# Kernel tuning notes

Hardware: AMD Instinct MI355X
Metric: run time of the kernel (lower is better)

The kernel has to match this reference:

```python
import jax, jax.numpy as jnp
import numpy as np

B, D, H = 8192, 256, 1024


def setup_inputs() -> dict:
    key = jax.random.key(0)
    ks = jax.random.split(key, 24)
    glorot = lambda k, o, i: jax.random.uniform(k, (o, i), jnp.float32, -1.0, 1.0) * jnp.sqrt(6.0 / (o + i))
    inp = {
        'x': jax.random.normal(ks[0], (B, D), jnp.float32),
        'm': (jax.random.uniform(ks[1], (B, D)) < 0.8).astype(jnp.float32),  # binary observation mask
        'delta': jax.random.uniform(ks[2], (B, D), jnp.float32),             # nonnegative time gaps
        'h': jax.random.normal(ks[3], (B, H), jnp.float32),
        'x_last_obs': jax.random.normal(ks[4], (B, D), jnp.float32),
        'x_mean': jax.random.normal(ks[5], (D,), jnp.float32),
        'W_gamma_x': jax.random.uniform(ks[6], (D,), jnp.float32, 0.001, 0.01),
        'b_gamma_x': jnp.zeros((D,), jnp.float32),
        'W_gamma_h': glorot(ks[7], H, D), 'b_gamma_h': jnp.zeros((H,), jnp.float32),
        'W_xz': glorot(ks[8], H, D), 'W_hz': glorot(ks[9], H, H),
        'W_mz': glorot(ks[10], H, D), 'b_mz': jnp.zeros((H,), jnp.float32),
        'W_xr': glorot(ks[11], H, D), 'W_hr': glorot(ks[12], H, H),
        'W_mr': glorot(ks[13], H, D), 'b_mr': jnp.zeros((H,), jnp.float32),
        'W_xh': glorot(ks[14], H, D), 'W_hh': glorot(ks[15], H, H),
        'W_mh': glorot(ks[16], H, D), 'b_mh': jnp.zeros((H,), jnp.float32),
    }
    return inp


def reference(x, m, delta, h, x_last_obs, x_mean,
              W_gamma_x, b_gamma_x, W_gamma_h, b_gamma_h,
              W_xz, W_hz, W_mz, b_mz,
              W_xr, W_hr, W_mr, b_mr,
              W_xh, W_hh, W_mh, b_mh):
    # input decay (per-feature) and hidden decay (linear of delta)
    gamma_x = jnp.exp(-jax.nn.relu(delta * W_gamma_x + b_gamma_x))        # [B, D]
    gamma_h = jnp.exp(-jax.nn.relu(delta @ W_gamma_h.T + b_gamma_h))     # [B, H]
    # imputation
    x_last_obs_new = jnp.where(m > 0, x, x_last_obs)
    x_imputed = gamma_x * x_last_obs_new + (1.0 - gamma_x) * x_mean
    x_hat = m * x + (1.0 - m) * x_imputed
    h_decayed = gamma_h * h
    # GRU gates (eval mode: no recurrent dropout)
    z = jax.nn.sigmoid(x_hat @ W_xz.T + h_decayed @ W_hz.T + m @ W_mz.T + b_mz)
    r = jax.nn.sigmoid(x_hat @ W_xr.T + h_decayed @ W_hr.T + m @ W_mr.T + b_mr)
    h_tilde = jnp.tanh(x_hat @ W_xh.T + (r * h_decayed) @ W_hh.T + m @ W_mh.T + b_mh)
    h_new = (1.0 - z) * h_decayed + z * h_tilde
    return h_new, x_last_obs_new
```

## Files before the change

kernel.cpp:

```cpp
#include <hip/hip_runtime.h>
#include <cstdint>
#include <cstddef>

typedef unsigned short u16;
typedef __attribute__((ext_vector_type(8))) short s16x8;
typedef __attribute__((ext_vector_type(8))) u16 u16x8;
typedef __attribute__((ext_vector_type(4))) float f32x4;

#define DEV static __device__ __forceinline__
#define GPTR(p) (const __attribute__((address_space(1))) void*)(p)
#define LPTR(p) (__attribute__((address_space(3))) void*)(p)
#define SCHEDB __builtin_amdgcn_sched_barrier(0)
#define BAR __builtin_amdgcn_s_barrier()
#define SETP1 __builtin_amdgcn_s_setprio(1)
#define SETP0 __builtin_amdgcn_s_setprio(0)

DEV float b2f(u16 u) { union { unsigned i; float f; } c; c.i = ((unsigned)u) << 16; return c.f; }
DEV u16 f2b(float f) {
  union { float f; unsigned i; } c; c.f = f;
  unsigned r = (c.i + 0x7fffu + ((c.i >> 16) & 1u)) >> 16;
  return (u16)r;
}
DEV float sigm(float x) { return 1.0f / (1.0f + __expf(-x)); }

__global__ __launch_bounds__(256) void pack_w(
    const float* __restrict__ Wxz, const float* __restrict__ Whz, const float* __restrict__ Wmz,
    const float* __restrict__ Wxr, const float* __restrict__ Whr, const float* __restrict__ Wmr,
    const float* __restrict__ Wxh, const float* __restrict__ Whh, const float* __restrict__ Wmh,
    const float* __restrict__ Wgh,
    u16* __restrict__ WZR, u16* __restrict__ WH, u16* __restrict__ WGH)
{
  int t = blockIdx.x * 256 + threadIdx.x;
  const float* src;
  u16* dst;
  if (t < 589824) {
    int row = t / 192;
    int col = (t % 192) * 8;
    int rr = row & 1023;
    const float *wx, *wh, *wm;
    if (row < 1024)      { wx = Wxz; wh = Whz; wm = Wmz; }
    else if (row < 2048) { wx = Wxr; wh = Whr; wm = Wmr; }
    else                 { wx = Wxh; wh = Whh; wm = Wmh; }
    if (col < 256)       src = wx + rr * 256 + col;
    else if (col < 1280) src = wh + (size_t)rr * 1024 + (col - 256);
    else                 src = wm + rr * 256 + (col - 1280);
    dst = (row < 2048) ? (WZR + (size_t)row * 1536 + col)
                       : (WH + (size_t)(row - 2048) * 1536 + col);
  } else {
    int t2 = t - 589824;
    src = Wgh + t2 * 8;
    dst = WGH + t2 * 8;
  }
  f32x4 a = *(const f32x4*)src;
  f32x4 b = *(const f32x4*)(src + 4);
  u16x8 v;
#pragma unroll
  for (int j = 0; j < 4; ++j) { v[j] = f2b(a[j]); v[j + 4] = f2b(b[j]); }
  *(u16x8*)dst = v;
}

__global__ __launch_bounds__(256) void elem_k(
    const float* __restrict__ x, const float* __restrict__ m, const float* __restrict__ delta,
    const float* __restrict__ xlo, const float* __restrict__ x_mean,
    const float* __restrict__ Wgx, const float* __restrict__ bgx,
    u16* __restrict__ X1, u16* __restrict__ X2, u16* __restrict__ Dbf,
    float* __restrict__ out_xlo)
{
  int t = blockIdx.x * 256 + threadIdx.x;
  int row = t >> 5;
  int col = (t & 31) * 8;
  size_t base = (size_t)row * 256 + col;
  u16x8 vxhat, vm16, vd16;
  f32x4 vlnew[2];
#pragma unroll
  for (int half = 0; half < 2; ++half) {
    f32x4 vx = *(const f32x4*)(x + base + half * 4);
    f32x4 vm = *(const f32x4*)(m + base + half * 4);
    f32x4 vd = *(const f32x4*)(delta + base + half * 4);
    f32x4 vl = *(const f32x4*)(xlo + base + half * 4);
    f32x4 vmean = *(const f32x4*)(x_mean + col + half * 4);
    f32x4 vwg = *(const f32x4*)(Wgx + col + half * 4);
    f32x4 vbg = *(const f32x4*)(bgx + col + half * 4);
#pragma unroll
    for (int j = 0; j < 4; ++j) {
      float mf = vm[j];
      float lnew = (mf > 0.5f) ? vx[j] : vl[j];
      vlnew[half][j] = lnew;
      float gx = __expf(-fmaxf(vd[j] * vwg[j] + vbg[j], 0.0f));
      float ximp = gx * lnew + (1.0f - gx) * vmean[j];
      float xhat = mf * vx[j] + (1.0f - mf) * ximp;
      vxhat[half * 4 + j] = f2b(xhat);
      vm16[half * 4 + j] = f2b(mf);
      vd16[half * 4 + j] = f2b(vd[j]);
    }
  }
  size_t r1536 = (size_t)row * 1536;
  *(u16x8*)(X1 + r1536 + col) = vxhat;
  *(u16x8*)(X2 + r1536 + col) = vxhat;
  *(u16x8*)(X1 + r1536 + 1280 + col) = vm16;
  *(u16x8*)(X2 + r1536 + 1280 + col) = vm16;
  *(u16x8*)(Dbf + base) = vd16;
  *(f32x4*)(out_xlo + base) = vlnew[0];
  *(f32x4*)(out_xlo + base + 4) = vlnew[1];
}

template<int EPI, int GXL>
__global__ __launch_bounds__(512, 4) void gemm_bt(
    const u16* __restrict__ A, int K, const u16* __restrict__ W,
    const float* __restrict__ bias0, const float* __restrict__ bias1,
    const float* __restrict__ auxf,
    const u16* __restrict__ auxb,
    const u16* __restrict__ aux2b,
    u16* __restrict__ out0b,
    u16* __restrict__ out1b,
    float* __restrict__ outf)
{
  constexpr int GX = 1 << GXL;
  constexpr int SL = 128 * 32;
  __shared__ alignas(16) u16 As[4][SL];
  __shared__ alignas(16) u16 Bs[4][SL];

  const int tid = threadIdx.x;
  const int lane = tid & 63;
  const int wave = tid >> 6;
  const int wr = wave >> 2, wc = wave & 3;

  const int d = blockIdx.x;
  const int q = (int)gridDim.x >> 3;
  const int L = (d & 7) * q + (d >> 3);
  const int brow = (L >> GXL) * 128;
  const int bcol = (L & (GX - 1)) * 128;
  const int NT = K / 64;

  const int lr = lane & 15, g4 = lane >> 4;
  const int rc = (g4 ^ ((lr >> 1) & 3)) * 8;
  const int srow = lane >> 2;
  const int scs = ((lane & 3) ^ ((srow >> 1) & 3)) * 8;

  f32x4 acc[4][2];
#pragma unroll
  for (int i = 0; i < 4; ++i)
#pragma unroll
    for (int j = 0; j < 2; ++j) { f32x4 z0 = {0.f, 0.f, 0.f, 0.f}; acc[i][j] = z0; }

  const u16* aP = A + (size_t)(brow + wave * 16 + srow) * K + scs;
  const u16* bP = W + (size_t)(bcol + wave * 16 + srow) * K + scs;
  u16* ldsA = &As[0][0] + wave * 512;
  u16* ldsB = &Bs[0][0] + wave * 512;
  const u16* rdA = &As[0][0] + (wr * 64 + lr) * 32 + rc;
  const u16* rdB = &Bs[0][0] + (wc * 32 + lr) * 32 + rc;

  auto STAGE = [&](int slot, int koff) {
    __builtin_amdgcn_global_load_lds(GPTR(aP + koff), LPTR(ldsA + slot * SL), 16, 0, 0);
    __builtin_amdgcn_global_load_lds(GPTR(bP + koff), LPTR(ldsB + slot * SL), 16, 0, 0);
  };

  auto PHASE = [&](int slotR, int slotS, int koff, int stg, int vm) {
    s16x8 af[4], bf[2];
    const u16* pA = rdA + slotR * SL;
    const u16* pB = rdB + slotR * SL;
#pragma unroll
    for (int i = 0; i < 4; ++i) af[i] = *(const s16x8*)(pA + i * 512);
#pragma unroll
    for (int j = 0; j < 2; ++j) bf[j] = *(const s16x8*)(pB + j * 512);
    if (stg) STAGE(slotS, koff);
    SCHEDB;
    if (vm == 2) asm volatile("s_waitcnt vmcnt(2)" ::: "memory");
    else if (vm == 0) asm volatile("s_waitcnt vmcnt(0)" ::: "memory");
    BAR;
    asm volatile("s_waitcnt lgkmcnt(0)" ::: "memory");
    SCHEDB;
    SETP1;
#pragma unroll
    for (int i = 0; i < 4; ++i)
#pragma unroll
      for (int j = 0; j < 2; ++j)
        acc[i][j] = __builtin_amdgcn_mfma_f32_16x16x32_bf16(af[i], bf[j], acc[i][j], 0, 0, 0);
    SETP0;
  };

  STAGE(0, 0);
  STAGE(1, 32);
  asm volatile("s_waitcnt vmcnt(2)" ::: "memory");
  BAR;

  for (int kt = 0; kt < NT - 2; kt += 2) {
    PHASE(0, 2, 64, 1, 2);
    PHASE(1, 3, 96, 1, 2);
    PHASE(2, 0, 128, 1, 2);
    PHASE(3, 1, 160, 1, 2);
    aP += 128; bP += 128;
  }
  PHASE(0, 2, 64, 1, 2);
  PHASE(1, 3, 96, 1, 2);
  PHASE(2, 0, 0, 0, 0);
  PHASE(3, 0, 0, 0, -1);

  const int row0 = brow + wr * 64 + g4 * 4;
  const int col0 = bcol + wc * 32 + lr;
#pragma unroll
  for (int i = 0; i < 4; ++i) {
#pragma unroll
    for (int j = 0; j < 2; ++j) {
      int c_ = col0 + j * 16;
#pragma unroll
      for (int qq = 0; qq < 4; ++qq) {
        int r_ = row0 + i * 16 + qq;
        float v = acc[i][j][qq];
        if constexpr (EPI == 0) {
          float p = v + bias0[c_];
          float gh = __expf(-fmaxf(p, 0.0f));
          float hd = gh * auxf[(size_t)r_ * 1024 + c_];
          out0b[(size_t)r_ * 1536 + 256 + c_] = f2b(hd);
        } else if constexpr (EPI == 1) {
          if (c_ < 1024) {
            out0b[(size_t)r_ * 1024 + c_] = f2b(sigm(v + bias0[c_]));
          } else {
            int jc = c_ - 1024;
            float rg = sigm(v + bias1[jc]);
            float hd = b2f(auxb[(size_t)r_ * 1536 + 256 + jc]);
            out1b[(size_t)r_ * 1536 + 256 + jc] = f2b(rg * hd);
          }
        } else {
          float ht = tanhf(v + bias0[c_]);
          float zz = b2f(aux2b[(size_t)r_ * 1024 + c_]);
          float hd = b2f(auxb[(size_t)r_ * 1536 + 256 + c_]);
          outf[(size_t)r_ * 1024 + c_] = (1.0f - zz) * hd + zz * ht;
        }
      }
    }
  }
}

extern "C" void kernel_launch(void* const* d_in, const int* in_sizes, int n_in,
                              void* d_out, int out_size, void* d_ws, size_t ws_size,
                              hipStream_t stream)
{
  const float* x     = (const float*)d_in[0];
  const float* m     = (const float*)d_in[1];
  const float* delta = (const float*)d_in[2];
  const float* h     = (const float*)d_in[3];
  const float* xlo   = (const float*)d_in[4];
  const float* xmean = (const float*)d_in[5];
  const float* Wgx   = (const float*)d_in[6];
  const float* bgx   = (const float*)d_in[7];
  const float* Wgh   = (const float*)d_in[8];
  const float* bgh   = (const float*)d_in[9];
  const float* Wxz   = (const float*)d_in[10];
  const float* Whz   = (const float*)d_in[11];
  const float* Wmz   = (const float*)d_in[12];
  const float* bmz   = (const float*)d_in[13];
  const float* Wxr   = (const float*)d_in[14];
  const float* Whr   = (const float*)d_in[15];
  const float* Wmr   = (const float*)d_in[16];
  const float* bmr   = (const float*)d_in[17];
  const float* Wxh   = (const float*)d_in[18];
  const float* Whh   = (const float*)d_in[19];
  const float* Wmh   = (const float*)d_in[20];
  const float* bmh   = (const float*)d_in[21];

  u16* X1  = (u16*)d_ws;
  u16* X2  = X1 + (size_t)8192 * 1536;
  u16* Z   = X2 + (size_t)8192 * 1536;
  u16* WZR = Z  + (size_t)8192 * 1024;
  u16* WH  = WZR + (size_t)2048 * 1536;
  u16* Dbf = WH + (size_t)1024 * 1536;
  u16* WGH = Dbf + (size_t)8192 * 256;

  float* out_h   = (float*)d_out;
  float* out_xlo = out_h + (size_t)8192 * 1024;

  pack_w<<<2432, 256, 0, stream>>>(Wxz, Whz, Wmz, Wxr, Whr, Wmr, Wxh, Whh, Wmh, Wgh, WZR, WH, WGH);
  elem_k<<<1024, 256, 0, stream>>>(x, m, delta, xlo, xmean, Wgx, bgx, X1, X2, Dbf, out_xlo);
  gemm_bt<0, 3><<<512, 512, 0, stream>>>(
      Dbf, 256, WGH, bgh, nullptr, h, nullptr, nullptr, X1, nullptr, nullptr);
  gemm_bt<1, 4><<<1024, 512, 0, stream>>>(
      X1, 1536, WZR, bmz, bmr, nullptr, X1, nullptr, Z, X2, nullptr);
  gemm_bt<2, 3><<<512, 512, 0, stream>>>(
      X2, 1536, WH, bmh, nullptr, nullptr, X1, Z, nullptr, nullptr, out_h);
}
```

Baseline: 159.8 us.

## Use 256x128 tiles with triple-buffered pipeline for the z/r gate GEMM

Replaces the generic 128x128 gate GEMM (z and r gates, K=1536, N=2048) with a dedicated kernel using 256x128 block tiles, 8 waves each computing a 64x64 sub-tile, a BK=32 triple-buffered direct global-to-LDS load pipeline and one barrier per step. Larger tiles give more MFMA work per loaded byte and halve the grid to 512 blocks. The old EPI==1 path and its extra output parameter are removed. The cost is higher register use (16 accumulators per wave) and a finer K step with more barriers, which could limit occupancy or latency hiding.

Measured after the change: 153.6 us (median of 2 runs). 1.04x faster.

```diff
diff --git a/kernel.cpp b/kernel.cpp
--- a/kernel.cpp
+++ b/kernel.cpp
@@ -104,6 +104,99 @@
   *(f32x4*)(out_xlo + base + 4) = vlnew[1];
 }
 
+__global__ __launch_bounds__(512, 4) void gemm_b256(
+    const u16* __restrict__ A, const u16* __restrict__ W,
+    const float* __restrict__ bz, const float* __restrict__ br,
+    const u16* __restrict__ X1h, u16* __restrict__ Z, u16* __restrict__ X2)
+{
+  constexpr int K = 1536, P = 48;
+  __shared__ alignas(16) u16 As[3][8192];
+  __shared__ alignas(16) u16 Bs[3][4096];
+
+  const int tid = threadIdx.x, lane = tid & 63, wave = tid >> 6;
+  const int wr = wave >> 1, wc = wave & 1;
+  const int d = blockIdx.x;
+  const int L = (d & 7) * 64 + (d >> 3);
+  const int brow = (L >> 4) * 256, bcol = (L & 15) * 128;
+  const int lr = lane & 15, g4 = lane >> 4;
+  const int rc = (g4 ^ ((lr >> 1) & 3)) * 8;
+  const int srow = tid >> 2;
+  const int scs = ((tid & 3) ^ ((srow >> 1) & 3)) * 8;
+
+  f32x4 acc[4][4];
+#pragma unroll
+  for (int i = 0; i < 4; ++i)
+#pragma unroll
+    for (int j = 0; j < 4; ++j) { f32x4 z0 = {0.f, 0.f, 0.f, 0.f}; acc[i][j] = z0; }
+
+  const u16* aP = A + (size_t)(brow + srow) * K + scs;
+  const u16* aQ = aP + (size_t)128 * K;
+  const u16* bP = W + (size_t)(bcol + srow) * K + scs;
+  u16* dA = &As[0][0] + tid * 8;
+  u16* dB = &Bs[0][0] + tid * 8;
+  const u16* rA = &As[0][0] + (wr * 64 + lr) * 32 + rc;
+  const u16* rB = &Bs[0][0] + (wc * 64 + lr) * 32 + rc;
+
+  auto STAGE = [&](int slot, int ko) {
+    __builtin_amdgcn_global_load_lds(GPTR(aP + ko), LPTR(dA + slot * 8192), 16, 0, 0);
+    __builtin_amdgcn_global_load_lds(GPTR(aQ + ko), LPTR(dA + slot * 8192 + 4096), 16, 0, 0);
+    __builtin_amdgcn_global_load_lds(GPTR(bP + ko), LPTR(dB + slot * 4096), 16, 0, 0);
+  };
+
+  STAGE(0, 0);
+  STAGE(1, 32);
+  asm volatile("s_waitcnt vmcnt(3)" ::: "memory");
+  BAR;
+
+#pragma unroll
+  for (int u = 0; u < P; ++u) {
+    const int sR = u % 3;
+    const int sS = (u + 2) % 3;
+    const int ko = ((u + 2 < P) ? (u + 2) : (P - 1)) * 32;
+    s16x8 af[4], bf[4];
+#pragma unroll
+    for (int i = 0; i < 4; ++i) af[i] = *(const s16x8*)(rA + sR * 8192 + i * 512);
+#pragma unroll
+    for (int j = 0; j < 4; ++j) bf[j] = *(const s16x8*)(rB + sR * 4096 + j * 512);
+    STAGE(sS, ko);
+    SCHEDB;
+    asm volatile("s_waitcnt vmcnt(3) lgkmcnt(0)" ::: "memory");
+    SCHEDB;
+    BAR;
+    SETP1;
+#pragma unroll
+    for (int i = 0; i < 4; ++i)
+#pragma unroll
+      for (int j = 0; j < 4; ++j)
+        acc[i][j] = __builtin_amdgcn_mfma_f32_16x16x32_bf16(af[i], bf[j], acc[i][j], 0, 0, 0);
+    SETP0;
+  }
+  asm volatile("s_waitcnt vmcnt(0)" ::: "memory");
+
+  const int row0 = brow + wr * 64 + g4 * 4;
+  const int col0 = bcol + wc * 64 + lr;
+#pragma unroll
+  for (int i = 0; i < 4; ++i) {
+#pragma unroll
+    for (int j = 0; j < 4; ++j) {
+      int c_ = col0 + j * 16;
+#pragma unroll
+      for (int qq = 0; qq < 4; ++qq) {
+        int r_ = row0 + i * 16 + qq;
+        float v = acc[i][j][qq];
+        if (c_ < 1024) {
+          Z[(size_t)r_ * 1024 + c_] = f2b(sigm(v + bz[c_]));
+        } else {
+          int jc = c_ - 1024;
+          float rg = sigm(v + br[jc]);
+          float hd = b2f(X1h[(size_t)r_ * 1536 + 256 + jc]);
+          X2[(size_t)r_ * 1536 + 256 + jc] = f2b(rg * hd);
+        }
+      }
+    }
+  }
+}
+
 template<int EPI, int GXL>
 __global__ __launch_bounds__(512, 4) void gemm_bt(
     const u16* __restrict__ A, int K, const u16* __restrict__ W,
@@ -112,7 +205,6 @@
     const u16* __restrict__ auxb,
     const u16* __restrict__ aux2b,
     u16* __restrict__ out0b,
-    u16* __restrict__ out1b,
     float* __restrict__ outf)
 {
   constexpr int GX = 1 << GXL;
@@ -212,15 +304,6 @@
           float gh = __expf(-fmaxf(p, 0.0f));
           float hd = gh * auxf[(size_t)r_ * 1024 + c_];
           out0b[(size_t)r_ * 1536 + 256 + c_] = f2b(hd);
-        } else if constexpr (EPI == 1) {
-          if (c_ < 1024) {
-            out0b[(size_t)r_ * 1024 + c_] = f2b(sigm(v + bias0[c_]));
-          } else {
-            int jc = c_ - 1024;
-            float rg = sigm(v + bias1[jc]);
-            float hd = b2f(auxb[(size_t)r_ * 1536 + 256 + jc]);
-            out1b[(size_t)r_ * 1536 + 256 + jc] = f2b(rg * hd);
-          }
         } else {
           float ht = tanhf(v + bias0[c_]);
           float zz = b2f(aux2b[(size_t)r_ * 1024 + c_]);
@@ -273,9 +356,8 @@
   pack_w<<<2432, 256, 0, stream>>>(Wxz, Whz, Wmz, Wxr, Whr, Wmr, Wxh, Whh, Wmh, Wgh, WZR, WH, WGH);
   elem_k<<<1024, 256, 0, stream>>>(x, m, delta, xlo, xmean, Wgx, bgx, X1, X2, Dbf, out_xlo);
   gemm_bt<0, 3><<<512, 512, 0, stream>>>(
-      Dbf, 256, WGH, bgh, nullptr, h, nullptr, nullptr, X1, nullptr, nullptr);
-  gemm_bt<1, 4><<<1024, 512, 0, stream>>>(
-      X1, 1536, WZR, bmz, bmr, nullptr, X1, nullptr, Z, X2, nullptr);
+      Dbf, 256, WGH, bgh, nullptr, h, nullptr, nullptr, X1, nullptr);
+  gemm_b256<<<512, 512, 0, stream>>>(X1, WZR, bmz, bmr, X1, Z, X2);
   gemm_bt<2, 3><<<512, 512, 0, stream>>>(
-      X2, 1536, WH, bmh, nullptr, nullptr, X1, Z, nullptr, nullptr, out_h);
-}
+      X2, 1536, WH, bmh, nullptr, nullptr, X1, Z, nullptr, out_h);
+}
```
